# Kernel tuning notes

Measured on AMD Instinct MI355X. Metric: run time of the kernel, lower is better.

The kernel has to match this reference:

```python
import jax, jax.numpy as jnp
import numpy as np

IN_SIZE = 256
OUT_SIZE = 256
WIN = 2  # window_size


def setup_inputs() -> dict:
    key = jax.random.key(0)
    k1, k2 = jax.random.split(key)
    x = jax.random.normal(k1, (8, 4096, IN_SIZE), dtype=jnp.float32)
    W = jax.random.normal(k2, (3 * OUT_SIZE, WIN * IN_SIZE), dtype=jnp.float32) * 0.05
    b = jnp.zeros((3 * OUT_SIZE,), dtype=jnp.float32)
    return {"x": x, "W": W, "b": b}


def reference(x, W, b):
    bsz, seq_len, _ = x.shape
    toks = [x]
    for i in range(WIN - 1):
        shifted = jnp.concatenate(
            [jnp.zeros((bsz, i + 1, IN_SIZE), x.dtype), x[:, : -(i + 1), :]], axis=1
        )
        toks.insert(0, shifted)
    xw = jnp.stack(toks, axis=2).reshape(bsz, seq_len, WIN * IN_SIZE)

    # Gated projection: z (update), f (forget), o (output)
    y = xw @ W.T + b  # (B, S, 3*OUT)
    z, f, o = jnp.split(y, 3, axis=2)
    z = jnp.tanh(z)
    f = jax.nn.sigmoid(f)

    # fo-pooling recurrence: c_t = f_t * c_{t-1} + (1 - f_t) * z_t
    def step(c, fz):
        ft, zt = fz
        c = ft * c + (1.0 - ft) * zt
        return c, c

    fz = (jnp.swapaxes(f, 0, 1), jnp.swapaxes(z, 0, 1))  # (S, B, OUT)
    c0 = jnp.zeros((bsz, OUT_SIZE), z.dtype)
    _, cs = jax.lax.scan(step, c0, fz)
    c = jnp.swapaxes(cs, 0, 1)  # (B, S, OUT)

    return jax.nn.sigmoid(o) * c
```

## Files before the change

kernel.cpp:

```cpp
#include <hip/hip_runtime.h>
#include <cstdint>
#include <cstddef>

#define BATCH  8
#define SEQ    4096
#define CHN    256
#define NQ     768
#define KTOT   512
#define S_B    128
#define TS     128
#define NCHUNK (SEQ/TS)

typedef __attribute__((ext_vector_type(8))) __bf16    bf16x8;
typedef __attribute__((ext_vector_type(4))) __bf16    bf16x4;
typedef __attribute__((ext_vector_type(4))) float     f32x4;
typedef __attribute__((ext_vector_type(4))) _Float16  f16x4;
typedef __attribute__((ext_vector_type(2))) _Float16  f16x2;

__global__ __launch_bounds__(256) void k_convW(const float* __restrict__ W,
                                               __bf16* __restrict__ Wt) {
    int lin = blockIdx.x * 256 + threadIdx.x;
    int n  = lin % NQ;
    int tg = lin / NQ;
    const float* src = W + (size_t)n * KTOT + tg * 8;
    float4 a = *(const float4*)(src);
    float4 b = *(const float4*)(src + 4);
    bf16x8 h;
    h[0]=(__bf16)a.x; h[1]=(__bf16)a.y; h[2]=(__bf16)a.z; h[3]=(__bf16)a.w;
    h[4]=(__bf16)b.x; h[5]=(__bf16)b.y; h[6]=(__bf16)b.z; h[7]=(__bf16)b.w;
    *(bf16x8*)(Wt + (size_t)lin * 8) = h;
}

__device__ __forceinline__ float fast_sigmoid(float y) {
    float e = __expf(-y);
    return __builtin_amdgcn_rcpf(1.f + e);
}
__device__ __forceinline__ float fast_tanh(float y) {
    float e = __expf(-2.f * y);
    return __builtin_amdgcn_rcpf(1.f + e) * 2.f - 1.f;
}

__global__ __launch_bounds__(512, 4) void k_gemm(
    const float* __restrict__ x, const __bf16* __restrict__ Wt,
    const float* __restrict__ bias,
    _Float16* __restrict__ Zb, _Float16* __restrict__ Fb, _Float16* __restrict__ Ob)
{
    __shared__ __bf16 As[(S_B + 1) * 256];

    int tid = threadIdx.x;
    int bid = blockIdx.x;
    int nsl  = bid % 3;
    int rest = bid / 3;
    int bi = rest >> 5;
    int sc = rest & 31;
    int s0 = sc * S_B;
    int wid = tid >> 6;
    int l   = tid & 63;
    int l15 = l & 15, lg = l >> 4;
    int wn = wid & 3;
    int ws = wid >> 2;

    for (int i = 0; i < 17; ++i) {
        int idx = tid + i * 512;
        if (idx < (S_B + 1) * 64) {
            int r  = idx >> 6, cg = idx & 63;
            int srow = s0 - 1 + r;
            float4 v = make_float4(0.f, 0.f, 0.f, 0.f);
            if (srow >= 0)
                v = *(const float4*)(x + ((size_t)bi * SEQ + srow) * CHN + cg * 4);
            bf16x4 h;
            h[0]=(__bf16)v.x; h[1]=(__bf16)v.y; h[2]=(__bf16)v.z; h[3]=(__bf16)v.w;
            int boff = (r * 512 + cg * 8) ^ ((r & 7) << 4);
            *(bf16x4*)((char*)As + boff) = h;
        }
    }
    __syncthreads();

    f32x4 acc[4][4];
    const f32x4 vzero = {0.f, 0.f, 0.f, 0.f};
    #pragma unroll
    for (int a = 0; a < 4; ++a)
        #pragma unroll
        for (int b = 0; b < 4; ++b)
            acc[a][b] = vzero;

    int nbase = nsl * 256 + wn * 64 + l15;
    const __bf16* wbase = Wt + ((size_t)lg * NQ + nbase) * 8;

    #pragma unroll
    for (int t = 0; t < 16; ++t) {
        int kh  = t >> 3;
        int kc0 = (t & 7) * 32;
        bf16x8 xf[4];
        #pragma unroll
        for (int st = 0; st < 4; ++st) {
            int row  = ws * 64 + st * 16 + l15 + kh;
            int boff = (row * 512 + kc0 * 2 + lg * 16) ^ ((row & 7) << 4);
            xf[st] = *(const bf16x8*)((const char*)As + boff);
        }
        bf16x8 wf[4];
        #pragma unroll
        for (int nt = 0; nt < 4; ++nt)
            wf[nt] = *(const bf16x8*)(wbase + ((size_t)t * 4 * NQ + nt * 16) * 8);
        #pragma unroll
        for (int nt = 0; nt < 4; ++nt)
            #pragma unroll
            for (int st = 0; st < 4; ++st)
                acc[nt][st] = __builtin_amdgcn_mfma_f32_16x16x32_bf16(
                                  wf[nt], xf[st], acc[nt][st], 0, 0, 0);
    }

    _Float16* buf = (nsl == 0) ? Zb : (nsl == 1) ? Fb : Ob;
    bool is_tanh = (nsl == 0);
    #pragma unroll
    for (int nt = 0; nt < 4; ++nt) {
        int chb = wn * 64 + nt * 16 + lg * 4;
        float4 bv = *(const float4*)(bias + nsl * 256 + chb);
        #pragma unroll
        for (int st = 0; st < 4; ++st) {
            int s = s0 + ws * 64 + st * 16 + l15;
            f16x4 h;
            #pragma unroll
            for (int r = 0; r < 4; ++r) {
                float bvr = (r == 0) ? bv.x : (r == 1) ? bv.y : (r == 2) ? bv.z : bv.w;
                float y = acc[nt][st][r] + bvr;
                float v = is_tanh ? fast_tanh(y) : fast_sigmoid(y);
                h[r] = (_Float16)v;
            }
            *(f16x4*)(buf + ((size_t)bi * SEQ + s) * CHN + chb) = h;
        }
    }
}

__global__ __launch_bounds__(128) void k_scan1(const _Float16* __restrict__ Fb,
                                               const _Float16* __restrict__ Zb,
                                               float* __restrict__ Aq,
                                               float* __restrict__ Bq) {
    int bi = blockIdx.x >> 5;
    int ck = blockIdx.x & 31;
    int c2 = threadIdx.x;
    size_t base = (((size_t)bi * SEQ + ck * TS) * CHN + c2 * 2) >> 1;
    const f16x2* F2 = (const f16x2*)Fb;
    const f16x2* Z2 = (const f16x2*)Zb;
    float a0 = 1.f, a1 = 1.f, c0 = 0.f, c1 = 0.f;
    #pragma unroll 8
    for (int s = 0; s < TS; ++s) {
        f16x2 f = F2[base + (size_t)s * (CHN / 2)];
        f16x2 z = Z2[base + (size_t)s * (CHN / 2)];
        float f0 = (float)f[0], f1 = (float)f[1];
        c0 = f0 * c0 + (1.f - f0) * (float)z[0];
        c1 = f1 * c1 + (1.f - f1) * (float)z[1];
        a0 *= f0; a1 *= f1;
    }
    int o = blockIdx.x * CHN + c2 * 2;
    *(float2*)(Aq + o) = make_float2(a0, a1);
    *(float2*)(Bq + o) = make_float2(c0, c1);
}

__global__ __launch_bounds__(256) void k_scan2(const float* __restrict__ Aq,
                                               const float* __restrict__ Bq,
                                               float* __restrict__ Cq) {
    int bi = blockIdx.x;
    int ch = threadIdx.x;
    float c = 0.f;
    #pragma unroll
    for (int ck = 0; ck < NCHUNK; ++ck) {
        int o = (bi * NCHUNK + ck) * CHN + ch;
        Cq[o] = c;
        c = Aq[o] * c + Bq[o];
    }
}

__global__ __launch_bounds__(128) void k_scan3(const _Float16* __restrict__ Fb,
                                               const _Float16* __restrict__ Zb,
                                               const _Float16* __restrict__ Ob,
                                               const float* __restrict__ Cq,
                                               float* __restrict__ out) {
    int bi = blockIdx.x >> 5;
    int ck = blockIdx.x & 31;
    int c2 = threadIdx.x;
    float2 c = *(const float2*)(Cq + blockIdx.x * CHN + c2 * 2);
    size_t base = (((size_t)bi * SEQ + ck * TS) * CHN + c2 * 2) >> 1;
    const f16x2* F2 = (const f16x2*)Fb;
    const f16x2* Z2 = (const f16x2*)Zb;
    const f16x2* O2 = (const f16x2*)Ob;
    float* outp = out + (((size_t)bi * SEQ + ck * TS) * CHN + c2 * 2);
    #pragma unroll 4
    for (int s = 0; s < TS; ++s) {
        f16x2 f  = F2[base + (size_t)s * (CHN / 2)];
        f16x2 z  = Z2[base + (size_t)s * (CHN / 2)];
        f16x2 so = O2[base + (size_t)s * (CHN / 2)];
        float f0 = (float)f[0], f1 = (float)f[1];
        c.x = f0 * c.x + (1.f - f0) * (float)z[0];
        c.y = f1 * c.y + (1.f - f1) * (float)z[1];
        *(float2*)(outp + (size_t)s * CHN) = make_float2((float)so[0] * c.x,
                                                         (float)so[1] * c.y);
    }
}

extern "C" void kernel_launch(void* const* d_in, const int* in_sizes, int n_in,
                              void* d_out, int out_size, void* d_ws, size_t ws_size,
                              hipStream_t stream)
{
    const float* x = (const float*)d_in[0];
    const float* W = (const float*)d_in[1];
    const float* b = (const float*)d_in[2];
    float* out = (float*)d_out;

    char* ws = (char*)d_ws;
    const size_t MB = 1024 * 1024;
    _Float16* Zb = (_Float16*)(ws +  0 * MB);
    _Float16* Fb = (_Float16*)(ws + 16 * MB);
    _Float16* Ob = (_Float16*)(ws + 32 * MB);
    __bf16*   Wt = (__bf16*)  (ws + 48 * MB);
    float*    Aq = (float*)   (ws + 49 * MB);
    float*    Bq = (float*)   (ws + 50 * MB);
    float*    Cq = (float*)   (ws + 51 * MB);

    k_convW<<<dim3(192),            dim3(256), 0, stream>>>(W, Wt);
    k_gemm <<<dim3(3 * BATCH * 32), dim3(512), 0, stream>>>(x, Wt, b, Zb, Fb, Ob);
    k_scan1<<<dim3(BATCH * NCHUNK), dim3(128), 0, stream>>>(Fb, Zb, Aq, Bq);
    k_scan2<<<dim3(BATCH),          dim3(256), 0, stream>>>(Aq, Bq, Cq);
    k_scan3<<<dim3(BATCH * NCHUNK), dim3(128), 0, stream>>>(Fb, Zb, Ob, Cq, out);
}
```

Baseline: 87.54 us.

## Restructure GEMM tiles to cover all gates per block and stage W via LDS

The GEMM block now computes all 768 output columns (z, f and o) for a 64-row sequence tile with 12 waves, instead of one gate slice per block. The x tile is therefore converted and loaded once rather than three times. Weight fragments are streamed into double-buffered LDS with global_load_lds, one k-step ahead. MFMA issue is wrapped in s_setprio. This trades a per-iteration barrier and larger LDS use, which limits occupancy, for less redundant x traffic and less direct global weight loading.

```diff
diff --git a/kernel.cpp b/kernel.cpp
--- a/kernel.cpp
+++ b/kernel.cpp
@@ -7,9 +7,12 @@
 #define CHN    256
 #define NQ     768
 #define KTOT   512
-#define S_B    128
+#define S_B    64
 #define TS     128
 #define NCHUNK (SEQ/TS)
+
+#define WPLANE 12320
+#define WBUF   (4*WPLANE)
 
 typedef __attribute__((ext_vector_type(8))) __bf16    bf16x8;
 typedef __attribute__((ext_vector_type(4))) __bf16    bf16x4;
@@ -40,28 +43,25 @@
     return __builtin_amdgcn_rcpf(1.f + e) * 2.f - 1.f;
 }
 
-__global__ __launch_bounds__(512, 4) void k_gemm(
+__global__ __launch_bounds__(768, 3) void k_gemm(
     const float* __restrict__ x, const __bf16* __restrict__ Wt,
     const float* __restrict__ bias,
     _Float16* __restrict__ Zb, _Float16* __restrict__ Fb, _Float16* __restrict__ Ob)
 {
-    __shared__ __bf16 As[(S_B + 1) * 256];
+    __shared__ char As_b[(S_B + 1) * 512];
+    __shared__ char Wl_b[2][WBUF];
 
     int tid = threadIdx.x;
-    int bid = blockIdx.x;
-    int nsl  = bid % 3;
-    int rest = bid / 3;
-    int bi = rest >> 5;
-    int sc = rest & 31;
-    int s0 = sc * S_B;
+    int bi  = blockIdx.x >> 6;
+    int sc  = blockIdx.x & 63;
+    int s0  = sc * S_B;
     int wid = tid >> 6;
     int l   = tid & 63;
     int l15 = l & 15, lg = l >> 4;
-    int wn = wid & 3;
-    int ws = wid >> 2;
-
-    for (int i = 0; i < 17; ++i) {
-        int idx = tid + i * 512;
+
+    #pragma unroll
+    for (int i = 0; i < 6; ++i) {
+        int idx = tid + i * 768;
         if (idx < (S_B + 1) * 64) {
             int r  = idx >> 6, cg = idx & 63;
             int srow = s0 - 1 + r;
@@ -71,9 +71,24 @@
             bf16x4 h;
             h[0]=(__bf16)v.x; h[1]=(__bf16)v.y; h[2]=(__bf16)v.z; h[3]=(__bf16)v.w;
             int boff = (r * 512 + cg * 8) ^ ((r & 7) << 4);
-            *(bf16x4*)((char*)As + boff) = h;
-        }
-    }
+            *(bf16x4*)(As_b + boff) = h;
+        }
+    }
+
+    const char* wt_lane = (const char*)Wt + ((size_t)wid * 64 + l) * 16;
+    #define STAGE_W(bufi, t)                                                     \
+        {                                                                        \
+            _Pragma("unroll")                                                    \
+            for (int g = 0; g < 4; ++g) {                                        \
+                const char* gsrc = wt_lane + (size_t)(t) * 49152 + g * 12288;    \
+                char* ldst = Wl_b[bufi] + g * WPLANE + wid * 1024;               \
+                __builtin_amdgcn_global_load_lds(                                \
+                    (const __attribute__((address_space(1))) void*)gsrc,         \
+                    (__attribute__((address_space(3))) void*)ldst, 16, 0, 0);    \
+            }                                                                    \
+        }
+
+    STAGE_W(0, 0);
     __syncthreads();
 
     f32x4 acc[4][4];
@@ -84,41 +99,48 @@
         for (int b = 0; b < 4; ++b)
             acc[a][b] = vzero;
 
-    int nbase = nsl * 256 + wn * 64 + l15;
-    const __bf16* wbase = Wt + ((size_t)lg * NQ + nbase) * 8;
-
     #pragma unroll
     for (int t = 0; t < 16; ++t) {
+        if (t < 15) STAGE_W((t + 1) & 1, t + 1);
+
         int kh  = t >> 3;
         int kc0 = (t & 7) * 32;
         bf16x8 xf[4];
         #pragma unroll
         for (int st = 0; st < 4; ++st) {
-            int row  = ws * 64 + st * 16 + l15 + kh;
+            int row  = st * 16 + l15 + kh;
             int boff = (row * 512 + kc0 * 2 + lg * 16) ^ ((row & 7) << 4);
-            xf[st] = *(const bf16x8*)((const char*)As + boff);
+            xf[st] = *(const bf16x8*)(As_b + boff);
         }
         bf16x8 wf[4];
         #pragma unroll
         for (int nt = 0; nt < 4; ++nt)
-            wf[nt] = *(const bf16x8*)(wbase + ((size_t)t * 4 * NQ + nt * 16) * 8);
+            wf[nt] = *(const bf16x8*)(Wl_b[t & 1] + lg * WPLANE +
+                                      (wid * 64 + nt * 16 + l15) * 16);
+
+        __builtin_amdgcn_s_setprio(1);
         #pragma unroll
         for (int nt = 0; nt < 4; ++nt)
             #pragma unroll
             for (int st = 0; st < 4; ++st)
                 acc[nt][st] = __builtin_amdgcn_mfma_f32_16x16x32_bf16(
                                   wf[nt], xf[st], acc[nt][st], 0, 0, 0);
-    }
-
-    _Float16* buf = (nsl == 0) ? Zb : (nsl == 1) ? Fb : Ob;
-    bool is_tanh = (nsl == 0);
+        __builtin_amdgcn_s_setprio(0);
+
+        if (t < 15) __syncthreads();
+    }
+
+    int gate = wid >> 2;
+    _Float16* buf = (gate == 0) ? Zb : (gate == 1) ? Fb : Ob;
+    bool is_tanh = (gate == 0);
     #pragma unroll
     for (int nt = 0; nt < 4; ++nt) {
-        int chb = wn * 64 + nt * 16 + lg * 4;
-        float4 bv = *(const float4*)(bias + nsl * 256 + chb);
+        int n4  = wid * 64 + nt * 16 + lg * 4;
+        int chn = n4 & 255;
+        float4 bv = *(const float4*)(bias + n4);
         #pragma unroll
         for (int st = 0; st < 4; ++st) {
-            int s = s0 + ws * 64 + st * 16 + l15;
+            int s = s0 + st * 16 + l15;
             f16x4 h;
             #pragma unroll
             for (int r = 0; r < 4; ++r) {
@@ -127,7 +149,7 @@
                 float v = is_tanh ? fast_tanh(y) : fast_sigmoid(y);
                 h[r] = (_Float16)v;
             }
-            *(f16x4*)(buf + ((size_t)bi * SEQ + s) * CHN + chb) = h;
+            *(f16x4*)(buf + ((size_t)bi * SEQ + s) * CHN + chn) = h;
         }
     }
 }
@@ -218,7 +240,7 @@
     float*    Cq = (float*)   (ws + 51 * MB);
 
     k_convW<<<dim3(192),            dim3(256), 0, stream>>>(W, Wt);
-    k_gemm <<<dim3(3 * BATCH * 32), dim3(512), 0, stream>>>(x, Wt, b, Zb, Fb, Ob);
+    k_gemm <<<dim3(BATCH * 64),     dim3(768), 0, stream>>>(x, Wt, b, Zb, Fb, Ob);
     k_scan1<<<dim3(BATCH * NCHUNK), dim3(128), 0, stream>>>(Fb, Zb, Aq, Bq);
     k_scan2<<<dim3(BATCH),          dim3(256), 0, stream>>>(Aq, Bq, Cq);
     k_scan3<<<dim3(BATCH * NCHUNK), dim3(128), 0, stream>>>(Fb, Zb, Ob, Cq, out);
```

New measurement: 88.23 us. Within noise of the previous version (+0.8%).

## Pre-convert x to padded bf16 buffer and stream GEMM operands from global

Applied to the files above, without the earlier changes.

Adds a separate kernel that converts x to bf16 once, into a per-batch buffer with a leading zero row that provides the shifted window. The GEMM no longer stages x in LDS; each wave loads both operands directly from global memory with register double-buffering across the K loop. Smaller 64-row tiles give more blocks. The epilogue transposes results through LDS so fp16 outputs are written as row-contiguous stores. The cost is an extra launch plus a bf16 x round trip, and each X fragment is re-read from global (or cache) by all three N-slice blocks.

```diff
diff --git a/kernel.cpp b/kernel.cpp
--- a/kernel.cpp
+++ b/kernel.cpp
@@ -7,12 +7,11 @@
 #define CHN    256
 #define NQ     768
 #define KTOT   512
-#define S_B    128
 #define TS     128
 #define NCHUNK (SEQ/TS)
+#define SROW   4097
 
 typedef __attribute__((ext_vector_type(8))) __bf16    bf16x8;
-typedef __attribute__((ext_vector_type(4))) __bf16    bf16x4;
 typedef __attribute__((ext_vector_type(4))) float     f32x4;
 typedef __attribute__((ext_vector_type(4))) _Float16  f16x4;
 typedef __attribute__((ext_vector_type(2))) _Float16  f16x2;
@@ -31,6 +30,27 @@
     *(bf16x8*)(Wt + (size_t)lin * 8) = h;
 }
 
+__global__ __launch_bounds__(256) void k_convX(const float* __restrict__ x,
+                                               __bf16* __restrict__ Xb) {
+    int c = blockIdx.x * 256 + threadIdx.x;
+    if (c < 8 * 32) {
+        int bz = c >> 5, j = c & 31;
+        bf16x8 zz = {};
+        *(bf16x8*)(Xb + (size_t)bz * SROW * 256 + j * 8) = zz;
+    }
+    int bi = c >> 17;
+    int r  = c & 131071;
+    int s  = r >> 5;
+    int j  = r & 31;
+    const float* src = x + ((size_t)bi * SEQ + s) * 256 + j * 8;
+    float4 a = *(const float4*)(src);
+    float4 b = *(const float4*)(src + 4);
+    bf16x8 h;
+    h[0]=(__bf16)a.x; h[1]=(__bf16)a.y; h[2]=(__bf16)a.z; h[3]=(__bf16)a.w;
+    h[4]=(__bf16)b.x; h[5]=(__bf16)b.y; h[6]=(__bf16)b.z; h[7]=(__bf16)b.w;
+    *(bf16x8*)(Xb + ((size_t)bi * SROW + 1 + s) * 256 + j * 8) = h;
+}
+
 __device__ __forceinline__ float fast_sigmoid(float y) {
     float e = __expf(-y);
     return __builtin_amdgcn_rcpf(1.f + e);
@@ -40,41 +60,40 @@
     return __builtin_amdgcn_rcpf(1.f + e) * 2.f - 1.f;
 }
 
-__global__ __launch_bounds__(512, 4) void k_gemm(
-    const float* __restrict__ x, const __bf16* __restrict__ Wt,
+__global__ __launch_bounds__(256, 3) void k_gemm(
+    const __bf16* __restrict__ Xb, const __bf16* __restrict__ Wt,
     const float* __restrict__ bias,
     _Float16* __restrict__ Zb, _Float16* __restrict__ Fb, _Float16* __restrict__ Ob)
 {
-    __shared__ __bf16 As[(S_B + 1) * 256];
+    __shared__ char Ep[4][8192];
 
     int tid = threadIdx.x;
     int bid = blockIdx.x;
-    int nsl  = bid % 3;
-    int rest = bid / 3;
-    int bi = rest >> 5;
-    int sc = rest & 31;
-    int s0 = sc * S_B;
+    int nb  = bid >> 9;
+    int bi  = (bid >> 6) & 7;
+    int sb  = bid & 63;
+    int s0  = sb * 64;
     int wid = tid >> 6;
     int l   = tid & 63;
     int l15 = l & 15, lg = l >> 4;
-    int wn = wid & 3;
-    int ws = wid >> 2;
-
-    for (int i = 0; i < 17; ++i) {
-        int idx = tid + i * 512;
-        if (idx < (S_B + 1) * 64) {
-            int r  = idx >> 6, cg = idx & 63;
-            int srow = s0 - 1 + r;
-            float4 v = make_float4(0.f, 0.f, 0.f, 0.f);
-            if (srow >= 0)
-                v = *(const float4*)(x + ((size_t)bi * SEQ + srow) * CHN + cg * 4);
-            bf16x4 h;
-            h[0]=(__bf16)v.x; h[1]=(__bf16)v.y; h[2]=(__bf16)v.z; h[3]=(__bf16)v.w;
-            int boff = (r * 512 + cg * 8) ^ ((r & 7) << 4);
-            *(bf16x4*)((char*)As + boff) = h;
-        }
-    }
-    __syncthreads();
+    int nbase = nb * 256 + wid * 64;
+
+    const __bf16* wp = Wt + (size_t)lg * 6144 + (nbase + l15) * 8;
+    const __bf16* xp = Xb + ((size_t)bi * SROW + s0 + l15) * 256 + lg * 8;
+
+    #define LOADW(dst, t)                                                        \
+        { _Pragma("unroll")                                                      \
+          for (int nt = 0; nt < 4; ++nt)                                         \
+              dst[nt] = *(const bf16x8*)(wp + (size_t)(t) * 24576 + nt * 128); }
+    #define LOADX(dst, t)                                                        \
+        { _Pragma("unroll")                                                      \
+          for (int st = 0; st < 4; ++st)                                         \
+              dst[st] = *(const bf16x8*)(xp + (size_t)(st * 16 + ((t) >> 3)) * 256 \
+                                            + ((t) & 7) * 32); }
+
+    bf16x8 wf[2][4], xf[2][4];
+    LOADW(wf[0], 0);
+    LOADX(xf[0], 0);
 
     f32x4 acc[4][4];
     const f32x4 vzero = {0.f, 0.f, 0.f, 0.f};
@@ -84,51 +103,45 @@
         for (int b = 0; b < 4; ++b)
             acc[a][b] = vzero;
 
-    int nbase = nsl * 256 + wn * 64 + l15;
-    const __bf16* wbase = Wt + ((size_t)lg * NQ + nbase) * 8;
-
     #pragma unroll
     for (int t = 0; t < 16; ++t) {
-        int kh  = t >> 3;
-        int kc0 = (t & 7) * 32;
-        bf16x8 xf[4];
-        #pragma unroll
-        for (int st = 0; st < 4; ++st) {
-            int row  = ws * 64 + st * 16 + l15 + kh;
-            int boff = (row * 512 + kc0 * 2 + lg * 16) ^ ((row & 7) << 4);
-            xf[st] = *(const bf16x8*)((const char*)As + boff);
-        }
-        bf16x8 wf[4];
-        #pragma unroll
-        for (int nt = 0; nt < 4; ++nt)
-            wf[nt] = *(const bf16x8*)(wbase + ((size_t)t * 4 * NQ + nt * 16) * 8);
+        int cur = t & 1, nxt = cur ^ 1;
+        if (t < 15) { LOADW(wf[nxt], t + 1); LOADX(xf[nxt], t + 1); }
         #pragma unroll
         for (int nt = 0; nt < 4; ++nt)
             #pragma unroll
             for (int st = 0; st < 4; ++st)
                 acc[nt][st] = __builtin_amdgcn_mfma_f32_16x16x32_bf16(
-                                  wf[nt], xf[st], acc[nt][st], 0, 0, 0);
-    }
-
-    _Float16* buf = (nsl == 0) ? Zb : (nsl == 1) ? Fb : Ob;
-    bool is_tanh = (nsl == 0);
+                                  wf[cur][nt], xf[cur][st], acc[nt][st], 0, 0, 0);
+    }
+
+    char* Lw = Ep[wid];
     #pragma unroll
     for (int nt = 0; nt < 4; ++nt) {
-        int chb = wn * 64 + nt * 16 + lg * 4;
-        float4 bv = *(const float4*)(bias + nsl * 256 + chb);
+        float4 bv = *(const float4*)(bias + nbase + nt * 16 + lg * 4);
         #pragma unroll
         for (int st = 0; st < 4; ++st) {
-            int s = s0 + ws * 64 + st * 16 + l15;
             f16x4 h;
             #pragma unroll
             for (int r = 0; r < 4; ++r) {
                 float bvr = (r == 0) ? bv.x : (r == 1) ? bv.y : (r == 2) ? bv.z : bv.w;
                 float y = acc[nt][st][r] + bvr;
-                float v = is_tanh ? fast_tanh(y) : fast_sigmoid(y);
+                float v = (nb == 0) ? fast_tanh(y) : fast_sigmoid(y);
                 h[r] = (_Float16)v;
             }
-            *(f16x4*)(buf + ((size_t)bi * SEQ + s) * CHN + chb) = h;
+            int byte = ((st * 16 + l15) * 128 + (nt * 16 + lg * 4) * 2)
+                       ^ ((l15 & 7) << 4);
+            *(f16x4*)(Lw + byte) = h;
         }
+    }
+    _Float16* buf = (nb == 0) ? Zb : (nb == 1) ? Fb : Ob;
+    int chb = wid * 64;
+    #pragma unroll
+    for (int so = 0; so < 16; ++so) {
+        int s_loc = so * 4 + (l >> 4);
+        int byte = (s_loc * 128 + (l & 15) * 8) ^ ((s_loc & 7) << 4);
+        f16x4 v = *(const f16x4*)(Lw + byte);
+        *(f16x4*)(buf + ((size_t)bi * SEQ + s0 + s_loc) * CHN + chb + (l & 15) * 4) = v;
     }
 }
 
@@ -216,9 +229,11 @@
     float*    Aq = (float*)   (ws + 49 * MB);
     float*    Bq = (float*)   (ws + 50 * MB);
     float*    Cq = (float*)   (ws + 51 * MB);
+    __bf16*   Xb = (__bf16*)  (ws + 52 * MB);
 
     k_convW<<<dim3(192),            dim3(256), 0, stream>>>(W, Wt);
-    k_gemm <<<dim3(3 * BATCH * 32), dim3(512), 0, stream>>>(x, Wt, b, Zb, Fb, Ob);
+    k_convX<<<dim3(4096),           dim3(256), 0, stream>>>(x, Xb);
+    k_gemm <<<dim3(1536),           dim3(256), 0, stream>>>(Xb, Wt, b, Zb, Fb, Ob);
     k_scan1<<<dim3(BATCH * NCHUNK), dim3(128), 0, stream>>>(Fb, Zb, Aq, Bq);
     k_scan2<<<dim3(BATCH),          dim3(256), 0, stream>>>(Aq, Bq, Cq);
     k_scan3<<<dim3(BATCH * NCHUNK), dim3(128), 0, stream>>>(Fb, Zb, Ob, Cq, out);
```

New measurement: 110.3 us. 26.0% more time.
